# Optimization experiments

Measured on AMD Instinct MI355X. Metric: run time of the kernel, lower is better.

The kernel has to match this reference:

```python
import jax, jax.numpy as jnp
import numpy as np

HIDDEN = 2048
HEADS = 32
GROUPS = 8
HEAD_DIM = HIDDEN // HEADS  # 64
BSZ = 1
SEQ = 2048
KV_DIM = GROUPS * HEAD_DIM  # 512


def setup_inputs() -> dict:
    key = jax.random.key(0)
    ks = jax.random.split(key, 10)
    scale = 1.0 / np.sqrt(HIDDEN)
    x = jax.random.normal(ks[0], (BSZ, SEQ, HIDDEN), dtype=jnp.float32)
    # causal mask: 1 where attention is disallowed (strictly upper triangular)
    causal_mask = jnp.triu(jnp.ones((SEQ, SEQ), dtype=jnp.float32), k=1)
    Wq = jax.random.normal(ks[1], (HIDDEN, HIDDEN), dtype=jnp.float32) * scale
    bq = jnp.zeros((HIDDEN,), dtype=jnp.float32)
    Wk = jax.random.normal(ks[2], (HIDDEN, KV_DIM), dtype=jnp.float32) * scale
    bk = jnp.zeros((KV_DIM,), dtype=jnp.float32)
    Wv = jax.random.normal(ks[3], (HIDDEN, KV_DIM), dtype=jnp.float32) * scale
    bv = jnp.zeros((KV_DIM,), dtype=jnp.float32)
    Wo = jax.random.normal(ks[4], (HIDDEN, HIDDEN), dtype=jnp.float32) * scale
    bo = jnp.zeros((HIDDEN,), dtype=jnp.float32)
    return {"x": x, "causal_mask": causal_mask, "Wq": Wq, "bq": bq,
            "Wk": Wk, "bk": bk, "Wv": Wv, "bv": bv, "Wo": Wo, "bo": bo}


def reference(x, causal_mask, Wq, bq, Wk, bk, Wv, bv, Wo, bo):
    b, s, _ = x.shape
    r = HEADS // GROUPS  # queries per KV group
    # projections
    q = (x @ Wq + bq).reshape(b, s, HEADS, HEAD_DIM).transpose(0, 2, 1, 3)   # [b,H,s,d]
    k = (x @ Wk + bk).reshape(b, s, GROUPS, HEAD_DIM).transpose(0, 2, 1, 3)  # [b,G,s,d]
    v = (x @ Wv + bv).reshape(b, s, GROUPS, HEAD_DIM).transpose(0, 2, 1, 3)  # [b,G,s,d]
    # group query heads: head h belongs to group h // r (matches torch expand/reshape order)
    qg = q.reshape(b, GROUPS, r, s, HEAD_DIM)
    inv_sqrt_d = 1.0 / jnp.sqrt(jnp.float32(HEAD_DIM))
    # scores without physically expanding K/V across heads
    scores = jnp.einsum('bgrsd,bgtd->bgrst', qg, k) * inv_sqrt_d  # [b,G,r,s,t]
    scores = scores + causal_mask * (-1e9)
    attn = jax.nn.softmax(scores, axis=-1)
    out = jnp.einsum('bgrst,bgtd->bgrsd', attn, v)                 # [b,G,r,s,d]
    out = out.reshape(b, HEADS, s, HEAD_DIM).transpose(0, 2, 1, 3).reshape(b, s, HIDDEN)
    return out @ Wo + bo
```

## Files before the change

kernel.cpp:

```cpp
#include <hip/hip_runtime.h>

typedef __attribute__((ext_vector_type(8))) short short8;
typedef __attribute__((ext_vector_type(4))) float f32x4;
typedef unsigned short us4 __attribute__((ext_vector_type(4)));
typedef unsigned int u32x2 __attribute__((ext_vector_type(2)));

#define S_LEN 2048
#define HID   2048
#define KVD   512
#define NH    32
#define NG    8
#define HD    64

__device__ __forceinline__ float b2f(ushort u) {
  union { uint i; float f; } c; c.i = ((uint)u) << 16; return c.f;
}
__device__ __forceinline__ ushort f2b(float f) {
  union { float f; uint u; } c; c.f = f;
  uint u = c.u;
  uint r = (u + 0x7FFFu + ((u >> 16) & 1u)) >> 16;
  return (ushort)r;
}

__global__ __launch_bounds__(256) void detect_dtype(
    const uint* __restrict__ mask, int* __restrict__ flagp)
{
  __shared__ int s_f32;
  if (threadIdx.x == 0) s_f32 = 1;
  __syncthreads();
  int bad = 0;
  for (int i = threadIdx.x; i < 8192; i += 256) {
    const uint w = mask[i];
    if (w != 0u && w != 0x3F800000u) bad = 1;
  }
  if (bad) s_f32 = 0;
  __syncthreads();
  if (threadIdx.x == 0) *flagp = s_f32;
}

__global__ __launch_bounds__(256) void convert_x(
    const void* __restrict__ src, ushort* __restrict__ dst, int n,
    const int* __restrict__ flagp)
{
  const int i = (blockIdx.x * 256 + threadIdx.x) * 4;
  if (i >= n) return;
  if (*flagp) {
    const f32x4 v = *(const f32x4*)((const float*)src + i);
    us4 o;
    o.x = f2b(v.x); o.y = f2b(v.y); o.z = f2b(v.z); o.w = f2b(v.w);
    *(us4*)(dst + i) = o;
  } else {
    *(us4*)(dst + i) = *(const us4*)((const ushort*)src + i);
  }
}

__global__ __launch_bounds__(256) void transpose_any(
    const void* __restrict__ src, ushort* __restrict__ dst, int R, int C,
    const int* __restrict__ flagp)
{
  const int f32 = *flagp;
  __shared__ ushort tile[32][33];
  const int x  = blockIdx.x * 32 + threadIdx.x;
  const int y0 = blockIdx.y * 32;
  for (int i = threadIdx.y; i < 32; i += 8) {
    const size_t idx = (size_t)(y0 + i) * C + x;
    tile[i][threadIdx.x] = f32 ? f2b(((const float*)src)[idx])
                               : ((const ushort*)src)[idx];
  }
  __syncthreads();
  const int xo  = blockIdx.y * 32 + threadIdx.x;
  const int yo0 = blockIdx.x * 32;
  for (int i = threadIdx.y; i < 32; i += 8)
    dst[(size_t)(yo0 + i) * R + xo] = tile[threadIdx.x][i];
}

struct GemmRegions {
  const ushort* Bt[3];
  const void*   bias[3];
  void*         out[3];
  int   ldo[3];
  int   trans[3];
  int   outf32[3];
  float scale[3];
  int   colStart[3];
  int   colEnd[3];
};

__global__ __launch_bounds__(256) void gemm_bt_kernel(
    const ushort* __restrict__ A, int M, int K, GemmRegions rg,
    const int* __restrict__ flagp)
{
  __shared__ __align__(16) short As[128 * 32];
  __shared__ __align__(16) short Bs[128 * 32];

  const int tid  = threadIdx.x;
  const int wave = tid >> 6;
  const int lane = tid & 63;
  const int wm = wave & 1, wn = wave >> 1;
  const int quad = lane >> 4, l16 = lane & 15;

  const int rowBase = blockIdx.y * 128;
  const int colBase = blockIdx.x * 128;

  int ri = 0;
#pragma unroll
  for (int i = 0; i < 3; ++i)
    if (colBase >= rg.colStart[i] && colBase < rg.colEnd[i]) ri = i;

  const int colLocal0   = colBase - rg.colStart[ri];
  const ushort* BtBase  = rg.Bt[ri] + (size_t)colLocal0 * K;
  const void* bias      = rg.bias[ri];
  void* outp            = rg.out[ri];
  const int   ldo   = rg.ldo[ri];
  const int   trans = rg.trans[ri];
  const int   of32  = rg.outf32[ri];
  const float scale = rg.scale[ri];

  const int sRow = tid >> 2;
  const int sCol = (tid & 3) * 8;

  const ushort* a0 = A + (size_t)(rowBase + sRow) * K + sCol;
  const ushort* a1 = A + (size_t)(rowBase + sRow + 64) * K + sCol;
  const ushort* b0 = BtBase + (size_t)sRow * K + sCol;
  const ushort* b1 = BtBase + (size_t)(sRow + 64) * K + sCol;

  f32x4 acc[4][4] = {};

  for (int k0 = 0; k0 < K; k0 += 32) {
    __syncthreads();
    *(short8*)&As[sRow * 32 + sCol]        = *(const short8*)(a0 + k0);
    *(short8*)&As[(sRow + 64) * 32 + sCol] = *(const short8*)(a1 + k0);
    *(short8*)&Bs[sRow * 32 + sCol]        = *(const short8*)(b0 + k0);
    *(short8*)&Bs[(sRow + 64) * 32 + sCol] = *(const short8*)(b1 + k0);
    __syncthreads();

    short8 af[4], bf[4];
#pragma unroll
    for (int mi = 0; mi < 4; ++mi)
      af[mi] = *(const short8*)&As[(wm * 64 + mi * 16 + l16) * 32 + quad * 8];
#pragma unroll
    for (int ni = 0; ni < 4; ++ni)
      bf[ni] = *(const short8*)&Bs[(wn * 64 + ni * 16 + l16) * 32 + quad * 8];

#pragma unroll
    for (int mi = 0; mi < 4; ++mi)
#pragma unroll
      for (int ni = 0; ni < 4; ++ni)
        acc[mi][ni] = __builtin_amdgcn_mfma_f32_16x16x32_bf16(
            af[mi], bf[ni], acc[mi][ni], 0, 0, 0);
  }

  const int f32io = *flagp;

#pragma unroll
  for (int ni = 0; ni < 4; ++ni) {
    const int cl = wn * 64 + ni * 16 + l16;
    const float bv = f32io ? ((const float*)bias)[colLocal0 + cl]
                           : b2f(((const ushort*)bias)[colLocal0 + cl]);
#pragma unroll
    for (int mi = 0; mi < 4; ++mi) {
      const int row0 = rowBase + wm * 64 + mi * 16 + quad * 4;
#pragma unroll
      for (int r = 0; r < 4; ++r) {
        const float val = (acc[mi][ni][r] + bv) * scale;
        if (!trans) {
          const size_t off = (size_t)(row0 + r) * ldo + colLocal0 + cl;
          if (of32 && f32io) ((float*)outp)[off] = val;
          else               ((ushort*)outp)[off] = f2b(val);
        } else {
          ((ushort*)outp)[(size_t)(colLocal0 + cl) * M + row0 + r] = f2b(val);
        }
      }
    }
  }
}

#define PSTR 40

__global__ __launch_bounds__(256, 2) void attn_kernel(
    const ushort* __restrict__ Q, const ushort* __restrict__ Kb,
    const ushort* __restrict__ Vt, ushort* __restrict__ O)
{
  __shared__ __align__(16) short Pls[4][64 * PSTR];

  const int tid  = threadIdx.x;
  const int wave = tid >> 6;
  const int lane = tid & 63;
  const int quad = lane >> 4, l16 = lane & 15;

  const int h = blockIdx.y;
  const int g = h >> 2;
  const int qbase = blockIdx.x * 256 + wave * 64;

  short8 qfB[4][2];
#pragma unroll
  for (int qf = 0; qf < 4; ++qf) {
    const ushort* qr = Q + (size_t)(qbase + qf * 16 + l16) * HID + h * HD;
#pragma unroll
    for (int ks = 0; ks < 2; ++ks)
      qfB[qf][ks] = *(const short8*)(qr + ks * 32 + quad * 8);
  }

  short8 ones;
#pragma unroll
  for (int j = 0; j < 8; ++j) ones[j] = (short)0x3F80;

  f32x4 o_acc[4][4] = {};
  f32x4 l_acc[4] = {};

  short* pb = &Pls[wave][0];
  const int nfull = qbase >> 5;

  auto body = [&](int it, bool edge) {
    const int t0 = it * 32;

    short8 kA[2][2];
#pragma unroll
    for (int kt = 0; kt < 2; ++kt) {
      const ushort* kr = Kb + (size_t)(t0 + kt * 16 + l16) * KVD + g * HD;
#pragma unroll
      for (int ks = 0; ks < 2; ++ks)
        kA[kt][ks] = *(const short8*)(kr + ks * 32 + quad * 8);
    }

#pragma unroll
    for (int qf = 0; qf < 4; ++qf) {
#pragma unroll
      for (int kt = 0; kt < 2; ++kt) {
        f32x4 z = {};
        z = __builtin_amdgcn_mfma_f32_16x16x32_bf16(kA[kt][0], qfB[qf][0], z, 0, 0, 0);
        z = __builtin_amdgcn_mfma_f32_16x16x32_bf16(kA[kt][1], qfB[qf][1], z, 0, 0, 0);
        ushort p[4];
#pragma unroll
        for (int r = 0; r < 4; ++r) {
          float pv = __expf(z[r]);
          if (edge) {
            const int key = t0 + kt * 16 + quad * 4 + r;
            const int qq  = qbase + qf * 16 + l16;
            if (key > qq) pv = 0.f;
          }
          p[r] = f2b(pv);
        }
        u32x2 w;
        w.x = (uint)p[0] | ((uint)p[1] << 16);
        w.y = (uint)p[2] | ((uint)p[3] << 16);
        *(u32x2*)&pb[(qf * 16 + l16) * PSTR + kt * 16 + quad * 4] = w;
      }
    }

    asm volatile("s_waitcnt lgkmcnt(0)" ::: "memory");

    short8 vB[4];
#pragma unroll
    for (int df = 0; df < 4; ++df)
      vB[df] = *(const short8*)(Vt + (size_t)(g * 64 + df * 16 + l16) * S_LEN
                                + t0 + quad * 8);

#pragma unroll
    for (int qf = 0; qf < 4; ++qf) {
      const short8 pa = *(const short8*)&pb[(qf * 16 + l16) * PSTR + quad * 8];
      l_acc[qf] = __builtin_amdgcn_mfma_f32_16x16x32_bf16(pa, ones, l_acc[qf], 0, 0, 0);
#pragma unroll
      for (int df = 0; df < 4; ++df)
        o_acc[qf][df] = __builtin_amdgcn_mfma_f32_16x16x32_bf16(
            pa, vB[df], o_acc[qf][df], 0, 0, 0);
    }
  };

  for (int it = 0; it < nfull; ++it) body(it, false);
  body(nfull, true);
  body(nfull + 1, true);

#pragma unroll
  for (int qf = 0; qf < 4; ++qf) {
    f32x4 linv;
#pragma unroll
    for (int r = 0; r < 4; ++r) linv[r] = 1.f / l_acc[qf][r];
#pragma unroll
    for (int df = 0; df < 4; ++df)
#pragma unroll
      for (int r = 0; r < 4; ++r)
        O[(size_t)(qbase + qf * 16 + quad * 4 + r) * HID + h * HD + df * 16 + l16]
            = f2b(o_acc[qf][df][r] * linv[r]);
  }
}

extern "C" void kernel_launch(void* const* d_in, const int* in_sizes, int n_in,
                              void* d_out, int out_size, void* d_ws, size_t ws_size,
                              hipStream_t stream) {
  (void)in_sizes; (void)n_in; (void)out_size; (void)ws_size;

  int* flagp = (int*)d_ws;
  ushort* base = (ushort*)d_ws + 16;
  const int M4 = 2048 * 2048;
  const int M1 = 512 * 2048;

  ushort* xb  = base;
  ushort* Wqt = xb  + M4;
  ushort* Wkt = Wqt + M4;
  ushort* Wvt = Wkt + M1;
  ushort* Qb  = Wvt + M1;
  ushort* Kb  = Qb  + M4;
  ushort* Vt  = Kb  + M1;
  ushort* Ob  = Wqt;
  ushort* Wot = Qb;

  detect_dtype<<<1, 256, 0, stream>>>((const uint*)d_in[1], flagp);
  convert_x<<<M4 / 1024, 256, 0, stream>>>(d_in[0], xb, M4, flagp);

  dim3 tb(32, 8);
  transpose_any<<<dim3(64, 64), tb, 0, stream>>>(d_in[2], Wqt, 2048, 2048, flagp);
  transpose_any<<<dim3(16, 64), tb, 0, stream>>>(d_in[4], Wkt, 2048, 512, flagp);
  transpose_any<<<dim3(16, 64), tb, 0, stream>>>(d_in[6], Wvt, 2048, 512, flagp);

  GemmRegions rq;
  rq.Bt[0] = Wqt; rq.bias[0] = d_in[3]; rq.out[0] = Qb; rq.ldo[0] = 2048;
  rq.trans[0] = 0; rq.outf32[0] = 0; rq.scale[0] = 0.125f;
  rq.colStart[0] = 0;    rq.colEnd[0] = 2048;
  rq.Bt[1] = Wkt; rq.bias[1] = d_in[5]; rq.out[1] = Kb; rq.ldo[1] = 512;
  rq.trans[1] = 0; rq.outf32[1] = 0; rq.scale[1] = 1.0f;
  rq.colStart[1] = 2048; rq.colEnd[1] = 2560;
  rq.Bt[2] = Wvt; rq.bias[2] = d_in[7]; rq.out[2] = Vt; rq.ldo[2] = 0;
  rq.trans[2] = 1; rq.outf32[2] = 0; rq.scale[2] = 1.0f;
  rq.colStart[2] = 2560; rq.colEnd[2] = 3072;
  gemm_bt_kernel<<<dim3(3072 / 128, 2048 / 128), 256, 0, stream>>>(
      xb, 2048, 2048, rq, flagp);

  attn_kernel<<<dim3(2048 / 256, NH), 256, 0, stream>>>(Qb, Kb, Vt, Ob);

  transpose_any<<<dim3(64, 64), tb, 0, stream>>>(d_in[8], Wot, 2048, 2048, flagp);

  GemmRegions ro;
  ro.Bt[0] = Wot; ro.bias[0] = d_in[9]; ro.out[0] = d_out; ro.ldo[0] = 2048;
  ro.trans[0] = 0; ro.outf32[0] = 1; ro.scale[0] = 1.0f;
  ro.colStart[0] = 0; ro.colEnd[0] = 2048;
  for (int i = 1; i < 3; ++i) {
    ro.Bt[i] = Wot; ro.bias[i] = d_in[9]; ro.out[i] = d_out; ro.ldo[i] = 2048;
    ro.trans[i] = 0; ro.outf32[i] = 1; ro.scale[i] = 1.0f;
    ro.colStart[i] = 0; ro.colEnd[i] = 0;
  }
  gemm_bt_kernel<<<dim3(2048 / 128, 2048 / 128), 256, 0, stream>>>(
      Ob, 2048, 2048, ro, flagp);
}
```

Before: 352.4 us.

## Split attention keys across waves with LDS reduction; use direct global-to-LDS loads in GEMM

The attention kernel now uses 64-query tiles per block, with two waves per 32-query half splitting the key range by alternating 32-key chunks. Partial outputs and row sums are combined through LDS atomics before normalization and a vectorized store. Tile order is permuted across the 1024 blocks to balance the causal workload, and occupancy is raised to four blocks per CU. Separately, the GEMM staging loads switch to global_load_lds so data goes straight into shared memory without a register round-trip, at the cost of LDS atomic contention and an extra sync.

```diff
diff --git a/kernel.cpp b/kernel.cpp
--- a/kernel.cpp
+++ b/kernel.cpp
@@ -11,6 +11,13 @@
 #define NH    32
 #define NG    8
 #define HD    64
+
+typedef __attribute__((address_space(3))) unsigned int  lds_u32;
+typedef __attribute__((address_space(1))) unsigned int  glb_u32;
+
+__device__ __forceinline__ void glds16(const void* g, void* l) {
+  __builtin_amdgcn_global_load_lds((glb_u32*)g, (lds_u32*)l, 16, 0, 0);
+}
 
 __device__ __forceinline__ float b2f(ushort u) {
   union { uint i; float f; } c; c.i = ((uint)u) << 16; return c.f;
@@ -124,14 +131,19 @@
   const ushort* b0 = BtBase + (size_t)sRow * K + sCol;
   const ushort* b1 = BtBase + (size_t)(sRow + 64) * K + sCol;
 
+  short* asDst0 = &As[tid * 8];
+  short* asDst1 = &As[64 * 32 + tid * 8];
+  short* bsDst0 = &Bs[tid * 8];
+  short* bsDst1 = &Bs[64 * 32 + tid * 8];
+
   f32x4 acc[4][4] = {};
 
   for (int k0 = 0; k0 < K; k0 += 32) {
     __syncthreads();
-    *(short8*)&As[sRow * 32 + sCol]        = *(const short8*)(a0 + k0);
-    *(short8*)&As[(sRow + 64) * 32 + sCol] = *(const short8*)(a1 + k0);
-    *(short8*)&Bs[sRow * 32 + sCol]        = *(const short8*)(b0 + k0);
-    *(short8*)&Bs[(sRow + 64) * 32 + sCol] = *(const short8*)(b1 + k0);
+    glds16(a0 + k0, asDst0);
+    glds16(a1 + k0, asDst1);
+    glds16(b0 + k0, bsDst0);
+    glds16(b1 + k0, bsDst1);
     __syncthreads();
 
     short8 af[4], bf[4];
@@ -175,27 +187,39 @@
   }
 }
 
-#define PSTR 40
-
-__global__ __launch_bounds__(256, 2) void attn_kernel(
+#define PSTR 34
+
+__global__ __launch_bounds__(256, 4) void attn_kernel(
     const ushort* __restrict__ Q, const ushort* __restrict__ Kb,
     const ushort* __restrict__ Vt, ushort* __restrict__ O)
 {
-  __shared__ __align__(16) short Pls[4][64 * PSTR];
+  __shared__ __align__(16) short Pls[4][32 * PSTR];
+  __shared__ float Oacc[64][64];
+  __shared__ float lacc[64];
 
   const int tid  = threadIdx.x;
   const int wave = tid >> 6;
   const int lane = tid & 63;
   const int quad = lane >> 4, l16 = lane & 15;
 
-  const int h = blockIdx.y;
-  const int g = h >> 2;
-  const int qbase = blockIdx.x * 256 + wave * 64;
-
-  short8 qfB[4][2];
-#pragma unroll
-  for (int qf = 0; qf < 4; ++qf) {
-    const ushort* qr = Q + (size_t)(qbase + qf * 16 + l16) * HID + h * HD;
+  const int id   = (blockIdx.x * 341) & 1023;
+  const int tile = id >> 5;
+  const int h    = id & 31;
+  const int g    = h >> 2;
+
+  const int half  = wave >> 1;
+  const int split = wave & 1;
+  const int qb32  = tile * 64 + half * 32;
+  const int ntot  = (qb32 >> 5) + 1;
+
+  for (int i = tid; i < 64 * 64; i += 256) ((float*)Oacc)[i] = 0.f;
+  if (tid < 64) lacc[tid] = 0.f;
+  __syncthreads();
+
+  short8 qfB[2][2];
+#pragma unroll
+  for (int qf = 0; qf < 2; ++qf) {
+    const ushort* qr = Q + (size_t)(qb32 + qf * 16 + l16) * HID + h * HD;
 #pragma unroll
     for (int ks = 0; ks < 2; ++ks)
       qfB[qf][ks] = *(const short8*)(qr + ks * 32 + quad * 8);
@@ -205,14 +229,13 @@
 #pragma unroll
   for (int j = 0; j < 8; ++j) ones[j] = (short)0x3F80;
 
-  f32x4 o_acc[4][4] = {};
-  f32x4 l_acc[4] = {};
-
+  f32x4 o_acc[2][4] = {};
+  f32x4 l_acc[2] = {};
   short* pb = &Pls[wave][0];
-  const int nfull = qbase >> 5;
-
-  auto body = [&](int it, bool edge) {
+
+  for (int it = split; it < ntot; it += 2) {
     const int t0 = it * 32;
+    const bool edge = (it == ntot - 1);
 
     short8 kA[2][2];
 #pragma unroll
@@ -222,9 +245,14 @@
       for (int ks = 0; ks < 2; ++ks)
         kA[kt][ks] = *(const short8*)(kr + ks * 32 + quad * 8);
     }
-
-#pragma unroll
-    for (int qf = 0; qf < 4; ++qf) {
+    short8 vB[4];
+#pragma unroll
+    for (int df = 0; df < 4; ++df)
+      vB[df] = *(const short8*)(Vt + (size_t)(g * 64 + df * 16 + l16) * S_LEN
+                                + t0 + quad * 8);
+
+#pragma unroll
+    for (int qf = 0; qf < 2; ++qf) {
 #pragma unroll
       for (int kt = 0; kt < 2; ++kt) {
         f32x4 z = {};
@@ -236,7 +264,7 @@
           float pv = __expf(z[r]);
           if (edge) {
             const int key = t0 + kt * 16 + quad * 4 + r;
-            const int qq  = qbase + qf * 16 + l16;
+            const int qq  = qb32 + qf * 16 + l16;
             if (key > qq) pv = 0.f;
           }
           p[r] = f2b(pv);
@@ -250,14 +278,8 @@
 
     asm volatile("s_waitcnt lgkmcnt(0)" ::: "memory");
 
-    short8 vB[4];
-#pragma unroll
-    for (int df = 0; df < 4; ++df)
-      vB[df] = *(const short8*)(Vt + (size_t)(g * 64 + df * 16 + l16) * S_LEN
-                                + t0 + quad * 8);
-
-#pragma unroll
-    for (int qf = 0; qf < 4; ++qf) {
+#pragma unroll
+    for (int qf = 0; qf < 2; ++qf) {
       const short8 pa = *(const short8*)&pb[(qf * 16 + l16) * PSTR + quad * 8];
       l_acc[qf] = __builtin_amdgcn_mfma_f32_16x16x32_bf16(pa, ones, l_acc[qf], 0, 0, 0);
 #pragma unroll
@@ -265,23 +287,37 @@
         o_acc[qf][df] = __builtin_amdgcn_mfma_f32_16x16x32_bf16(
             pa, vB[df], o_acc[qf][df], 0, 0, 0);
     }
-  };
-
-  for (int it = 0; it < nfull; ++it) body(it, false);
-  body(nfull, true);
-  body(nfull + 1, true);
-
-#pragma unroll
-  for (int qf = 0; qf < 4; ++qf) {
-    f32x4 linv;
-#pragma unroll
-    for (int r = 0; r < 4; ++r) linv[r] = 1.f / l_acc[qf][r];
+  }
+
+#pragma unroll
+  for (int qf = 0; qf < 2; ++qf) {
+    const int row = half * 32 + qf * 16 + quad * 4;
 #pragma unroll
     for (int df = 0; df < 4; ++df)
 #pragma unroll
       for (int r = 0; r < 4; ++r)
-        O[(size_t)(qbase + qf * 16 + quad * 4 + r) * HID + h * HD + df * 16 + l16]
-            = f2b(o_acc[qf][df][r] * linv[r]);
+        atomicAdd(&Oacc[row + r][df * 16 + l16], o_acc[qf][df][r]);
+    if (l16 == 0)
+#pragma unroll
+      for (int r = 0; r < 4; ++r)
+        atomicAdd(&lacc[row + r], l_acc[qf][r]);
+  }
+  __syncthreads();
+
+  {
+    const int row = tid >> 2;
+    const int c0  = (tid & 3) * 16;
+    const float linv = 1.f / lacc[row];
+    const size_t obase = (size_t)(tile * 64 + row) * HID + h * HD + c0;
+#pragma unroll
+    for (int j = 0; j < 4; ++j) {
+      us4 o;
+      o.x = f2b(Oacc[row][c0 + j * 4 + 0] * linv);
+      o.y = f2b(Oacc[row][c0 + j * 4 + 1] * linv);
+      o.z = f2b(Oacc[row][c0 + j * 4 + 2] * linv);
+      o.w = f2b(Oacc[row][c0 + j * 4 + 3] * linv);
+      *(us4*)(O + obase + j * 4) = o;
+    }
   }
 }
 
@@ -326,7 +362,7 @@
   gemm_bt_kernel<<<dim3(3072 / 128, 2048 / 128), 256, 0, stream>>>(
       xb, 2048, 2048, rq, flagp);
 
-  attn_kernel<<<dim3(2048 / 256, NH), 256, 0, stream>>>(Qb, Kb, Vt, Ob);
+  attn_kernel<<<dim3(1024), 256, 0, stream>>>(Qb, Kb, Vt, Ob);
 
   transpose_any<<<dim3(64, 64), tb, 0, stream>>>(d_in[8], Wot, 2048, 2048, flagp);
 
```

After: 398.2 us. 13.0% more time.
